# Optimization experiments

Measured on AMD Instinct MI355X. Metric: run time of the kernel, lower is better.

The kernel has to match this reference:

```python
import jax, jax.numpy as jnp
import numpy as np

NUM_HEADS = 16
HEAD_SIZE = 64
N_EMBD = 1024
BLOCK_SIZE = 2048
B, T = 4, 2048


def setup_inputs() -> dict:
    key = jax.random.key(0)
    ks = jax.random.split(key, 6)
    scale = (N_EMBD * NUM_HEADS) ** (-0.5)
    x = jax.random.normal(ks[0], (B, T, N_EMBD), dtype=jnp.float32)
    Wk = jax.random.normal(ks[1], (NUM_HEADS, N_EMBD, HEAD_SIZE), dtype=jnp.float32) * scale
    Wq = jax.random.normal(ks[2], (NUM_HEADS, N_EMBD, HEAD_SIZE), dtype=jnp.float32) * scale
    Wv = jax.random.normal(ks[3], (NUM_HEADS, N_EMBD, HEAD_SIZE), dtype=jnp.float32) * scale
    proj_w = jax.random.normal(ks[4], (N_EMBD, N_EMBD), dtype=jnp.float32) * (N_EMBD ** -0.5)
    proj_b = jax.random.normal(ks[5], (N_EMBD,), dtype=jnp.float32) * 0.01
    return {"x": x, "Wk": Wk, "Wq": Wq, "Wv": Wv, "proj_w": proj_w, "proj_b": proj_b}


def reference(x, Wk, Wq, Wv, proj_w, proj_b):
    Bsz, Tlen, C = x.shape
    # per-head projections: x [b,t,c] @ W [h,c,d] -> [b,h,t,d]
    q = jnp.einsum('btc,hcd->bhtd', x, Wq)
    k = jnp.einsum('btc,hcd->bhtd', x, Wk)
    v = jnp.einsum('btc,hcd->bhtd', x, Wv)
    wei = jnp.einsum('bhtd,bhsd->bhts', q, k) * (HEAD_SIZE ** -0.5)
    causal = jnp.tril(jnp.ones((Tlen, Tlen), dtype=bool))  # [T,T]
    wei = jnp.where(causal[None, None, :, :], wei, -jnp.inf)
    wei = jax.nn.softmax(wei, axis=-1)
    out = jnp.einsum('bhts,bhsd->bhtd', wei, v)
    out = out.transpose(0, 2, 1, 3).reshape(Bsz, Tlen, NUM_HEADS * HEAD_SIZE)
    out = out @ proj_w.T + proj_b  # nn.Linear: x W^T + b
    return out
```

## Files before the change

### kernel.cpp

```cpp
#include <hip/hip_runtime.h>
#include <hip/hip_bf16.h>

#define BB 4
#define TT 2048
#define CC 1024
#define HH 16
#define DD 64
#define MM (BB * TT)
#define NN_QKV 3072

typedef __attribute__((ext_vector_type(8))) short short8;
typedef __attribute__((ext_vector_type(4))) short short4v;
typedef __attribute__((ext_vector_type(4))) int i32x4;
typedef __attribute__((ext_vector_type(4))) float f32x4;
typedef __attribute__((ext_vector_type(16))) float f32x16;

static __device__ __forceinline__ float exp2_hw(float x) {
  return __builtin_amdgcn_exp2f(x);
}

static __device__ __forceinline__ short f2bf(float f) {
  __hip_bfloat16 h = __float2bfloat16(f);
  short s;
  __builtin_memcpy(&s, &h, 2);
  return s;
}

static __device__ __forceinline__ unsigned int pack2rn(float a, float b) {
  unsigned int ua, ub;
  __builtin_memcpy(&ua, &a, 4);
  __builtin_memcpy(&ub, &b, 4);
  ua += 0x8000u;
  ub += 0x8000u;
  return (ua >> 16) | (ub & 0xFFFF0000u);
}

static __device__ __forceinline__ f32x16 zero16() {
  f32x16 z;
#pragma unroll
  for (int i = 0; i < 16; ++i) z[i] = 0.f;
  return z;
}

static __device__ __forceinline__ int swzv(int d) {
  return (((d & 7) ^ ((d >> 3) & 7)) << 4);
}

static __device__ __forceinline__ void gld16(const void* g, void* l) {
  __builtin_amdgcn_global_load_lds(
      (const __attribute__((address_space(1))) unsigned int*)g,
      (__attribute__((address_space(3))) unsigned int*)l, 16, 0, 0);
}

__global__ __launch_bounds__(256) void cvt8_kernel(const float* __restrict__ in,
                                                   short* __restrict__ out, int n8) {
  int i = blockIdx.x * 256 + threadIdx.x;
  if (i >= n8) return;
  const float4 a = ((const float4*)in)[i * 2];
  const float4 b = ((const float4*)in)[i * 2 + 1];
  short8 o;
  o[0] = f2bf(a.x); o[1] = f2bf(a.y); o[2] = f2bf(a.z); o[3] = f2bf(a.w);
  o[4] = f2bf(b.x); o[5] = f2bf(b.y); o[6] = f2bf(b.z); o[7] = f2bf(b.w);
  ((short8*)out)[i] = o;
}

__global__ __launch_bounds__(256) void cvtw_kernel(
    const float* __restrict__ Wq, const float* __restrict__ Wk,
    const float* __restrict__ Wv, short* __restrict__ Wt) {
  __shared__ float tile[64][65];
  const int tid = threadIdx.x;
  const int h = blockIdx.x;
  const int c0 = blockIdx.y * 64;
  const int sel = blockIdx.z;
  const float* W = (sel == 0) ? Wq : (sel == 1) ? Wk : Wv;

#pragma unroll
  for (int it = 0; it < 16; ++it) {
    int e = it * 256 + tid;
    int cc = e >> 6, d = e & 63;
    tile[d][cc] = W[((size_t)h * CC + c0 + cc) * DD + d];
  }
  __syncthreads();
#pragma unroll
  for (int it = 0; it < 16; ++it) {
    int e = it * 256 + tid;
    int d = e >> 6, cc = e & 63;
    Wt[((size_t)((sel * 16 + h) * 64 + d)) * CC + c0 + cc] = f2bf(tile[d][cc]);
  }
}

template <int MODE>
__global__ __launch_bounds__(256) void mfma_gemm_kernel(
    const short* __restrict__ A, const short* __restrict__ Bt,
    const float* __restrict__ bias,
    __hip_bfloat16* __restrict__ Oq, __hip_bfloat16* __restrict__ Ok,
    __hip_bfloat16* __restrict__ Ov, float* __restrict__ Of) {
  __shared__ __align__(16) short Als[128 * 32];
  __shared__ __align__(16) short Bls[128 * 32];

  const int tid = threadIdx.x;
  const int w = tid >> 6, l = tid & 63;
  const int lg = l >> 4, ll = l & 15;
  const int wr = w >> 1, wc = w & 1;
  const int m0 = blockIdx.x * 128;
  const int n0 = blockIdx.y * 128;

  const int row0 = tid >> 2, kc0 = (tid & 3) * 8;
  const int row1 = (tid + 256) >> 2, kc1 = (tid & 3) * 8;

  f32x4 acc[4][4] = {};

  for (int kt = 0; kt < CC; kt += 32) {
    __syncthreads();
    gld16(A + (size_t)(m0 + row0) * CC + kt + kc0, (char*)Als + w * 1024);
    gld16(A + (size_t)(m0 + row1) * CC + kt + kc1, (char*)Als + 4096 + w * 1024);
    gld16(Bt + (size_t)(n0 + row0) * CC + kt + kc0, (char*)Bls + w * 1024);
    gld16(Bt + (size_t)(n0 + row1) * CC + kt + kc1, (char*)Bls + 4096 + w * 1024);
    __syncthreads();

    short8 af[4], bfr[4];
#pragma unroll
    for (int i = 0; i < 4; ++i)
      af[i] = *(const short8*)&Als[(wr * 64 + i * 16 + ll) * 32 + lg * 8];
#pragma unroll
    for (int j = 0; j < 4; ++j)
      bfr[j] = *(const short8*)&Bls[(wc * 64 + j * 16 + ll) * 32 + lg * 8];
#pragma unroll
    for (int i = 0; i < 4; ++i)
#pragma unroll
      for (int j = 0; j < 4; ++j)
        acc[i][j] = __builtin_amdgcn_mfma_f32_16x16x32_bf16(af[i], bfr[j], acc[i][j], 0, 0, 0);
  }

  if (MODE == 0) {
    const int b = m0 >> 11;
#pragma unroll
    for (int j = 0; j < 4; ++j) {
      const int nbase = n0 + wc * 64 + j * 16;
      const int sel = nbase >> 10;
      const int h = (nbase >> 6) & 15;
      const int d = (nbase & 63) + ll;
      __hip_bfloat16* O = (sel == 0) ? Oq : (sel == 1) ? Ok : Ov;
      const float sc = (sel == 0) ? 0.18033688011112042f : 1.0f;
#pragma unroll
      for (int i = 0; i < 4; ++i) {
#pragma unroll
        for (int r = 0; r < 4; ++r) {
          const int t = (m0 + wr * 64 + i * 16 + lg * 4 + r) & (TT - 1);
          O[(((size_t)b * HH + h) * TT + t) * DD + d] = __float2bfloat16(acc[i][j][r] * sc);
        }
      }
    }
  } else {
#pragma unroll
    for (int j = 0; j < 4; ++j) {
      const int n = n0 + wc * 64 + j * 16 + ll;
      const float bv = bias[n];
#pragma unroll
      for (int i = 0; i < 4; ++i) {
#pragma unroll
        for (int r = 0; r < 4; ++r) {
          const int m = m0 + wr * 64 + i * 16 + lg * 4 + r;
          Of[(size_t)m * CC + n] = acc[i][j][r] + bv;
        }
      }
    }
  }
}

__global__ __launch_bounds__(512) void attn32_kernel(
    const __hip_bfloat16* __restrict__ qg, const __hip_bfloat16* __restrict__ kg,
    const __hip_bfloat16* __restrict__ vg, __hip_bfloat16* __restrict__ att) {
  __shared__ __align__(16) char LDS[34816];
  char* Ks = LDS;
  char* Vt0 = LDS + 16384;
  char* Vt1 = LDS + 24576;

  const int tid = threadIdx.x;
  const int w = tid >> 6, l = tid & 63;
  const int l31 = l & 31, hi = l >> 5;
  const int w4 = w & 3, g = w >> 2;

  const int flat = blockIdx.x;
  const int r_ = flat >> 6;
  const int qt = (r_ < 4) ? (15 - r_) : (r_ < 8) ? (r_ + 4)
               : (r_ < 12) ? (15 - r_) : (r_ - 12);
  const int hb = flat & 63;
  const int h = hb & 15, b = hb >> 4;
  const size_t base = ((size_t)b * HH + h) * TT * DD;

  const int q0w = qt * 128 + w4 * 32;
  const int myq = q0w + l31;

  const short* Kg = (const short*)kg + base;
  const short* Vg = (const short*)vg + base;
  const int kr = tid >> 3;
  const int kc = tid & 7;
  const int vs = tid >> 3;
  const int vd0 = (tid & 7) * 8;

  const short* Qp = (const short*)qg + base + (size_t)myq * DD;
  const short8 qf0 = *(const short8*)(Qp + 0 + hi * 8);
  const short8 qf1 = *(const short8*)(Qp + 16 + hi * 8);
  const short8 qf2 = *(const short8*)(Qp + 32 + hi * 8);
  const short8 qf3 = *(const short8*)(Qp + 48 + hi * 8);

  f32x16 o0 = zero16(), o1 = zero16();
  float lsum = 0.f;

  const int npair = qt + 1;

#pragma unroll 1
  for (int pt = 0; pt < npair; ++pt) {
    const int sb = pt * 128;

    gld16(Kg + (size_t)(sb + kr) * DD + ((kc ^ (kr & 7)) * 8), Ks + w * 1024);
    gld16(Kg + (size_t)(sb + kr + 64) * DD + ((kc ^ (kr & 7)) * 8),
          Ks + 8192 + w * 1024);
    const short8 va = *(const short8*)(Vg + (size_t)(sb + vs) * DD + vd0);
    const short8 vb = *(const short8*)(Vg + (size_t)(sb + 64 + vs) * DD + vd0);
#pragma unroll
    for (int e = 0; e < 8; ++e) {
      const int d = vd0 + e;
      *(short*)(Vt0 + d * 128 + ((vs * 2) ^ swzv(d))) = va[e];
      *(short*)(Vt1 + d * 128 + ((vs * 2) ^ swzv(d))) = vb[e];
    }
    __syncthreads();

    const int sbg = sb + g * 64;
    const char* Vtg = g ? Vt1 : Vt0;
#pragma unroll
    for (int ks = 0; ks < 2; ++ks) {
      const int sbh = sbg + ks * 32;
      if (sbh > q0w + 31) continue;

      const int krow = g * 64 + ks * 32 + l31;
      const char* Kr = Ks + krow * 128;
      const int rsz = (krow & 7) << 4;
      const short8 kf0 = *(const short8*)(Kr + ((0 * 32 + hi * 16) ^ rsz));
      const short8 kf1 = *(const short8*)(Kr + ((1 * 32 + hi * 16) ^ rsz));
      const short8 kf2 = *(const short8*)(Kr + ((2 * 32 + hi * 16) ^ rsz));
      const short8 kf3 = *(const short8*)(Kr + ((3 * 32 + hi * 16) ^ rsz));
      f32x16 sT = zero16();
      __builtin_amdgcn_s_setprio(1);
      sT = __builtin_amdgcn_mfma_f32_32x32x16_bf16(kf0, qf0, sT, 0, 0, 0);
      sT = __builtin_amdgcn_mfma_f32_32x32x16_bf16(kf1, qf1, sT, 0, 0, 0);
      sT = __builtin_amdgcn_mfma_f32_32x32x16_bf16(kf2, qf2, sT, 0, 0, 0);
      sT = __builtin_amdgcn_mfma_f32_32x32x16_bf16(kf3, qf3, sT, 0, 0, 0);
      __builtin_amdgcn_s_setprio(0);

      float p[16];
      if (sbh == q0w) {
#pragma unroll
        for (int r = 0; r < 16; ++r) {
          const int sg = sbh + (r & 3) + 8 * (r >> 2) + 4 * hi;
          p[r] = (sg > myq) ? -INFINITY : sT[r];
        }
      } else {
#pragma unroll
        for (int r = 0; r < 16; ++r) p[r] = sT[r];
      }

      float ps = 0.f;
#pragma unroll
      for (int r = 0; r < 16; ++r) {
        p[r] = exp2_hw(p[r]);
        ps += p[r];
      }
      lsum += ps;

      unsigned int W[4][2], X[4][2];
#pragma unroll
      for (int qd = 0; qd < 4; ++qd) {
        W[qd][0] = pack2rn(p[4 * qd + 0], p[4 * qd + 1]);
        W[qd][1] = pack2rn(p[4 * qd + 2], p[4 * qd + 3]);
        X[qd][0] = __shfl_xor((int)W[qd][0], 32);
        X[qd][1] = __shfl_xor((int)W[qd][1], 32);
      }

#pragma unroll
      for (int kst = 0; kst < 2; ++kst) {
        union { i32x4 i; short8 s; } A;
        A.i[0] = hi ? (int)X[2 * kst + 1][0] : (int)W[2 * kst][0];
        A.i[1] = hi ? (int)X[2 * kst + 1][1] : (int)W[2 * kst][1];
        A.i[2] = hi ? (int)W[2 * kst + 1][0] : (int)X[2 * kst][0];
        A.i[3] = hi ? (int)W[2 * kst + 1][1] : (int)X[2 * kst][1];
        const int kb = (ks * 32 + kst * 16 + hi * 8) * 2;
        const int r0 = l31, r1 = 32 + l31;
        const short8 vf0 = *(const short8*)(Vtg + r0 * 128 + (kb ^ swzv(r0)));
        const short8 vf1 = *(const short8*)(Vtg + r1 * 128 + (kb ^ swzv(r1)));
        __builtin_amdgcn_s_setprio(1);
        o0 = __builtin_amdgcn_mfma_f32_32x32x16_bf16(vf0, A.s, o0, 0, 0, 0);
        o1 = __builtin_amdgcn_mfma_f32_32x32x16_bf16(vf1, A.s, o1, 0, 0, 0);
        __builtin_amdgcn_s_setprio(0);
      }
    }
    __syncthreads();
  }

  lsum += __shfl_xor(lsum, 32);

  float* comb = (float*)LDS;
  const int idx17 = (w4 * 64 + l) * 17;
  if (g == 1) {
#pragma unroll
    for (int i = 0; i < 16; ++i) comb[idx17 + i] = o0[i];
    comb[idx17 + 16] = lsum;
  }
  __syncthreads();
  if (g == 0) {
#pragma unroll
    for (int i = 0; i < 16; ++i) o0[i] += comb[idx17 + i];
    lsum += comb[idx17 + 16];
  }
  __syncthreads();
  const int idx16 = (w4 * 64 + l) * 16;
  if (g == 1) {
#pragma unroll
    for (int i = 0; i < 16; ++i) comb[idx16 + i] = o1[i];
  }
  __syncthreads();
  if (g == 0) {
#pragma unroll
    for (int i = 0; i < 16; ++i) o1[i] += comb[idx16 + i];

    const float inv = 1.0f / lsum;
    short* orow = (short*)att + ((size_t)b * TT + myq) * CC + h * DD;
#pragma unroll
    for (int j = 0; j < 4; ++j) {
      short4v s0, s1;
#pragma unroll
      for (int i = 0; i < 4; ++i) {
        s0[i] = f2bf(o0[4 * j + i] * inv);
        s1[i] = f2bf(o1[4 * j + i] * inv);
      }
      *(short4v*)(orow + 8 * j + 4 * hi) = s0;
      *(short4v*)(orow + 32 + 8 * j + 4 * hi) = s1;
    }
  }
}

extern "C" void kernel_launch(void* const* d_in, const int* in_sizes, int n_in,
                              void* d_out, int out_size, void* d_ws, size_t ws_size,
                              hipStream_t stream) {
  const float* x  = (const float*)d_in[0];
  const float* Wk = (const float*)d_in[1];
  const float* Wq = (const float*)d_in[2];
  const float* Wv = (const float*)d_in[3];
  const float* pw = (const float*)d_in[4];
  const float* pb = (const float*)d_in[5];
  float* out = (float*)d_out;

  const size_t QE = (size_t)BB * HH * TT * DD;
  __hip_bfloat16* q   = (__hip_bfloat16*)d_ws;
  __hip_bfloat16* k   = q + QE;
  __hip_bfloat16* v   = k + QE;
  short* xbf          = (short*)(v + QE);
  __hip_bfloat16* att = (__hip_bfloat16*)xbf;
  short* Wt           = xbf + QE;
  short* pwbf         = Wt;

  cvt8_kernel<<<(MM * CC / 8 + 255) / 256, 256, 0, stream>>>(x, xbf, MM * CC / 8);
  cvtw_kernel<<<dim3(HH, CC / 64, 3), 256, 0, stream>>>(Wq, Wk, Wv, Wt);
  mfma_gemm_kernel<0><<<dim3(MM / 128, NN_QKV / 128), 256, 0, stream>>>(
      xbf, Wt, nullptr, q, k, v, nullptr);
  attn32_kernel<<<dim3(1024, 1, 1), 512, 0, stream>>>(q, k, v, att);
  cvt8_kernel<<<(CC * CC / 8 + 255) / 256, 256, 0, stream>>>(pw, pwbf, CC * CC / 8);
  mfma_gemm_kernel<1><<<dim3(MM / 128, CC / 128), 256, 0, stream>>>(
      (const short*)att, pwbf, pb, nullptr, nullptr, nullptr, out);
}
```

Before: 162.0 us.

## Rewrite QKV projection GEMM with 32x32 MFMA, K=64 tiles and swizzled LDS

Splits the templated GEMM into a dedicated QKV kernel and a projection kernel. The QKV kernel now stages 64-wide K slices into XOR-swizzled LDS, so each barrier pair covers twice the K depth and bank conflicts drop. It also switches to 32x32x16 bf16 MFMA with setprio around the MFMA block. This is meant to cut barrier overhead and LDS traffic, but it raises LDS use per block and uses a more scattered 32x32 output layout on writeback.

```diff
diff --git a/kernel.cpp b/kernel.cpp
--- a/kernel.cpp
+++ b/kernel.cpp
@@ -89,12 +89,90 @@
   }
 }
 
-template <int MODE>
-__global__ __launch_bounds__(256) void mfma_gemm_kernel(
+__global__ __launch_bounds__(256) void qkv32_kernel(
     const short* __restrict__ A, const short* __restrict__ Bt,
-    const float* __restrict__ bias,
     __hip_bfloat16* __restrict__ Oq, __hip_bfloat16* __restrict__ Ok,
-    __hip_bfloat16* __restrict__ Ov, float* __restrict__ Of) {
+    __hip_bfloat16* __restrict__ Ov) {
+  __shared__ __align__(16) char Als[128 * 128];
+  __shared__ __align__(16) char Bls[128 * 128];
+
+  const int tid = threadIdx.x;
+  const int w = tid >> 6, l = tid & 63;
+  const int l31 = l & 31, hi = l >> 5;
+  const int wr = w >> 1, wc = w & 1;
+  const int m0 = blockIdx.x * 128;
+  const int n0 = blockIdx.y * 128;
+
+  const int srow = tid >> 3;
+  const int schunk = tid & 7;
+  const int sswz = (schunk ^ (srow & 7)) * 8;
+
+  f32x16 acc[2][2];
+  acc[0][0] = zero16(); acc[0][1] = zero16();
+  acc[1][0] = zero16(); acc[1][1] = zero16();
+
+#pragma unroll 1
+  for (int kt = 0; kt < CC; kt += 64) {
+    __syncthreads();
+#pragma unroll
+    for (int i = 0; i < 4; ++i) {
+      gld16(A + (size_t)(m0 + i * 32 + srow) * CC + kt + sswz,
+            Als + i * 4096 + w * 1024);
+      gld16(Bt + (size_t)(n0 + i * 32 + srow) * CC + kt + sswz,
+            Bls + i * 4096 + w * 1024);
+    }
+    __syncthreads();
+
+#pragma unroll
+    for (int ks = 0; ks < 4; ++ks) {
+      const int c = ks * 2 + hi;
+      short8 af[2], bf[2];
+#pragma unroll
+      for (int mi = 0; mi < 2; ++mi) {
+        const int row = wr * 64 + mi * 32 + l31;
+        af[mi] = *(const short8*)(Als + row * 128 + ((c ^ (row & 7)) * 16));
+      }
+#pragma unroll
+      for (int ni = 0; ni < 2; ++ni) {
+        const int row = wc * 64 + ni * 32 + l31;
+        bf[ni] = *(const short8*)(Bls + row * 128 + ((c ^ (row & 7)) * 16));
+      }
+      __builtin_amdgcn_s_setprio(1);
+#pragma unroll
+      for (int mi = 0; mi < 2; ++mi)
+#pragma unroll
+        for (int ni = 0; ni < 2; ++ni)
+          acc[mi][ni] = __builtin_amdgcn_mfma_f32_32x32x16_bf16(
+              af[mi], bf[ni], acc[mi][ni], 0, 0, 0);
+      __builtin_amdgcn_s_setprio(0);
+    }
+  }
+
+  const int b = m0 >> 11;
+#pragma unroll
+  for (int ni = 0; ni < 2; ++ni) {
+    const int nbase = n0 + wc * 64 + ni * 32;
+    const int sel = nbase >> 10;
+    const int h = (nbase >> 6) & 15;
+    const int d = (nbase & 63) + l31;
+    __hip_bfloat16* O = (sel == 0) ? Oq : (sel == 1) ? Ok : Ov;
+    const float sc = (sel == 0) ? 0.18033688011112042f : 1.0f;
+#pragma unroll
+    for (int mi = 0; mi < 2; ++mi) {
+#pragma unroll
+      for (int r = 0; r < 16; ++r) {
+        const int m = m0 + wr * 64 + mi * 32 + (r & 3) + 8 * (r >> 2) + 4 * hi;
+        const int t = m & (TT - 1);
+        O[(((size_t)b * HH + h) * TT + t) * DD + d] =
+            __float2bfloat16(acc[mi][ni][r] * sc);
+      }
+    }
+  }
+}
+
+__global__ __launch_bounds__(256) void proj_gemm_kernel(
+    const short* __restrict__ A, const short* __restrict__ Bt,
+    const float* __restrict__ bias, float* __restrict__ Of) {
   __shared__ __align__(16) short Als[128 * 32];
   __shared__ __align__(16) short Bls[128 * 32];
 
@@ -132,37 +210,16 @@
         acc[i][j] = __builtin_amdgcn_mfma_f32_16x16x32_bf16(af[i], bfr[j], acc[i][j], 0, 0, 0);
   }
 
-  if (MODE == 0) {
-    const int b = m0 >> 11;
-#pragma unroll
-    for (int j = 0; j < 4; ++j) {
-      const int nbase = n0 + wc * 64 + j * 16;
-      const int sel = nbase >> 10;
-      const int h = (nbase >> 6) & 15;
-      const int d = (nbase & 63) + ll;
-      __hip_bfloat16* O = (sel == 0) ? Oq : (sel == 1) ? Ok : Ov;
-      const float sc = (sel == 0) ? 0.18033688011112042f : 1.0f;
-#pragma unroll
-      for (int i = 0; i < 4; ++i) {
-#pragma unroll
-        for (int r = 0; r < 4; ++r) {
-          const int t = (m0 + wr * 64 + i * 16 + lg * 4 + r) & (TT - 1);
-          O[(((size_t)b * HH + h) * TT + t) * DD + d] = __float2bfloat16(acc[i][j][r] * sc);
-        }
-      }
-    }
-  } else {
-#pragma unroll
-    for (int j = 0; j < 4; ++j) {
-      const int n = n0 + wc * 64 + j * 16 + ll;
-      const float bv = bias[n];
-#pragma unroll
-      for (int i = 0; i < 4; ++i) {
-#pragma unroll
-        for (int r = 0; r < 4; ++r) {
-          const int m = m0 + wr * 64 + i * 16 + lg * 4 + r;
-          Of[(size_t)m * CC + n] = acc[i][j][r] + bv;
-        }
+#pragma unroll
+  for (int j = 0; j < 4; ++j) {
+    const int n = n0 + wc * 64 + j * 16 + ll;
+    const float bv = bias[n];
+#pragma unroll
+    for (int i = 0; i < 4; ++i) {
+#pragma unroll
+      for (int r = 0; r < 4; ++r) {
+        const int m = m0 + wr * 64 + i * 16 + lg * 4 + r;
+        Of[(size_t)m * CC + n] = acc[i][j][r] + bv;
       }
     }
   }
@@ -362,10 +419,10 @@
 
   cvt8_kernel<<<(MM * CC / 8 + 255) / 256, 256, 0, stream>>>(x, xbf, MM * CC / 8);
   cvtw_kernel<<<dim3(HH, CC / 64, 3), 256, 0, stream>>>(Wq, Wk, Wv, Wt);
-  mfma_gemm_kernel<0><<<dim3(MM / 128, NN_QKV / 128), 256, 0, stream>>>(
-      xbf, Wt, nullptr, q, k, v, nullptr);
+  qkv32_kernel<<<dim3(MM / 128, NN_QKV / 128), 256, 0, stream>>>(
+      xbf, Wt, q, k, v);
   attn32_kernel<<<dim3(1024, 1, 1), 512, 0, stream>>>(q, k, v, att);
   cvt8_kernel<<<(CC * CC / 8 + 255) / 256, 256, 0, stream>>>(pw, pwbf, CC * CC / 8);
-  mfma_gemm_kernel<1><<<dim3(MM / 128, CC / 128), 256, 0, stream>>>(
-      (const short*)att, pwbf, pb, nullptr, nullptr, nullptr, out);
-}
+  proj_gemm_kernel<<<dim3(MM / 128, CC / 128), 256, 0, stream>>>(
+      (const short*)att, pwbf, pb, out);
+}
```

New measurement: 160.1 us. No clear change (-1.1%).
